# Performance work log

Measured on AMD Instinct MI355X. Metric: run time of the kernel, lower is better.

Reference implementation:

```python
import jax, jax.numpy as jnp
import numpy as np

B, T, D = 4, 2048, 768
H, HD = 8, 96          # n_heads, head_dim
NB = HD // 24          # number of 24-dim Leech blocks per head
NEG_INF = -1e30


def _leech_kernel_24():
    # QR of the bidiagonal/circulant base matrix, as in generate_leech_kernel
    base = np.zeros((24, 24), dtype=np.float32)
    for i in range(23):
        base[i, i] = 2.0
        base[i, i + 1] = 2.0
    base[23, 23] = 2.0
    base[23, 0] = -2.0
    q, _ = np.linalg.qr(base)
    return jnp.asarray(q, dtype=jnp.float32)


def setup_inputs() -> dict:
    key = jax.random.key(0)
    k1, k2, k3 = jax.random.split(key, 3)
    x = jax.random.normal(k1, (B, T, D), dtype=jnp.float32)
    w_qkv = jax.random.normal(k2, (3 * D, D), dtype=jnp.float32) * (D ** -0.5)
    w_out = jax.random.normal(k3, (D, D), dtype=jnp.float32) * (D ** -0.5)
    kernel = _leech_kernel_24()
    return {"x": x, "w_qkv": w_qkv, "w_out": w_out, "kernel": kernel}


def reference(x, w_qkv, w_out, kernel):
    Bx, Tx, Dx = x.shape
    scale = HD ** -0.5
    # qkv projection (bias=False)
    qkv = jnp.einsum('btd,ed->bte', x, w_qkv)            # [B,T,3D]
    qkv = qkv.reshape(Bx, Tx, 3, H, HD).transpose(2, 0, 3, 1, 4)  # [3,B,H,T,HD]
    q, k, v = qkv[0], qkv[1], qkv[2]
    # per-24-block orthogonal Leech rotation on q and k
    q = jnp.einsum('bhtni,ij->bhtnj', q.reshape(Bx, H, Tx, NB, 24), kernel)
    k = jnp.einsum('bhtni,ij->bhtnj', k.reshape(Bx, H, Tx, NB, 24), kernel)
    q = q.reshape(Bx, H, Tx, HD)
    k = k.reshape(Bx, H, Tx, HD)
    # causal attention (manual softmax; dropout inactive in eval)
    scores = jnp.einsum('bhqd,bhkd->bhqk', q, k) * scale
    causal = jnp.tril(jnp.ones((Tx, Tx), dtype=bool))
    scores = jnp.where(causal[None, None], scores, NEG_INF)
    attn = jax.nn.softmax(scores, axis=-1)
    out = jnp.einsum('bhqk,bhkd->bhqd', attn, v)          # [B,H,T,HD]
    out = out.transpose(0, 2, 1, 3).reshape(Bx, Tx, Dx)
    return jnp.einsum('btd,ed->bte', out, w_out)
```

## Files before the change

kernel.cpp:

```cpp
#include <hip/hip_runtime.h>
#include <cstdint>
#include <cstddef>

#define Bq 4
#define T 2048
#define Dm 768
#define H 8
#define HD 96
#define BH 32
#define QEL ((size_t)BH*T*HD)
#define KEL ((size_t)BH*T*128)
#define PSTRIDE 98304
#define QS 0.14724703336f
#define KVB 64
#define M0 12.0f

typedef unsigned int u32;
typedef unsigned long long u64;
typedef _Float16 f16x8 __attribute__((ext_vector_type(8)));
typedef _Float16 f16x4 __attribute__((ext_vector_type(4)));
typedef float f32x4 __attribute__((ext_vector_type(4)));

__global__ __launch_bounds__(256)
void cvt_tile(const float* __restrict__ in, _Float16* __restrict__ out)
{
    const int tid  = threadIdx.x;
    const int lane = tid & 63;
    const int gw   = (blockIdx.x * 256 + tid) >> 6;
    const int kc   = gw % 96;
    const int row  = (gw / 96) * 64 + lane;
    const float4 a = *reinterpret_cast<const float4*>(in + (size_t)row * 768 + kc * 8);
    const float4 b = *reinterpret_cast<const float4*>(in + (size_t)row * 768 + kc * 8 + 4);
    f16x8 h;
    h[0] = (_Float16)a.x; h[1] = (_Float16)a.y; h[2] = (_Float16)a.z; h[3] = (_Float16)a.w;
    h[4] = (_Float16)b.x; h[5] = (_Float16)b.y; h[6] = (_Float16)b.z; h[7] = (_Float16)b.w;
    *reinterpret_cast<f16x8*>(
        out + (size_t)(row >> 7) * PSTRIDE + (size_t)kc * 1024 + (row & 127) * 8) = h;
}

template <bool SCATTER>
__global__ __launch_bounds__(256)
void gemm_mfma(const _Float16* __restrict__ At, const _Float16* __restrict__ Bt,
               _Float16* __restrict__ qb, _Float16* __restrict__ kpd,
               _Float16* __restrict__ vtb, float* __restrict__ C,
               int N, int nx)
{
    __shared__ _Float16 As[8 * 128 * 8];
    __shared__ _Float16 Bs[8 * 128 * 8];

    const int tid  = threadIdx.x;
    const int lane = tid & 63;
    const int wid  = tid >> 6;
    const int li   = lane & 15;
    const int lg   = lane >> 4;
    const int wr   = wid >> 1;
    const int wc   = wid & 1;

    const int qch = gridDim.x >> 3;
    const int id  = (blockIdx.x & 7) * qch + (blockIdx.x >> 3);
    const int m0  = (id / nx) * 128;
    const int n0  = (id % nx) * 128;

    const _Float16* baseA = At + (size_t)(m0 >> 7) * PSTRIDE;
    const _Float16* baseB = Bt + (size_t)(n0 >> 7) * PSTRIDE;

    f32x4 acc[4][4];
#pragma unroll
    for (int i = 0; i < 4; ++i)
#pragma unroll
        for (int j = 0; j < 4; ++j) acc[i][j] = (f32x4)0.f;

    for (int k0 = 0; k0 < Dm; k0 += 64) {
        const _Float16* pa = baseA + (k0 >> 3) * 1024;
        const _Float16* pb = baseB + (k0 >> 3) * 1024;
#pragma unroll
        for (int i = 0; i < 4; ++i) {
            const int s = wid * 64 + i * 256;
            __builtin_amdgcn_global_load_lds(
                (const __attribute__((address_space(1))) void*)(pa + (size_t)(s + lane) * 8),
                (__attribute__((address_space(3))) void*)&As[s * 8], 16, 0, 0);
            __builtin_amdgcn_global_load_lds(
                (const __attribute__((address_space(1))) void*)(pb + (size_t)(s + lane) * 8),
                (__attribute__((address_space(3))) void*)&Bs[s * 8], 16, 0, 0);
        }
        __syncthreads();

#pragma unroll
        for (int c = 0; c < 2; ++c) {
            f16x8 af[4], bf[4];
#pragma unroll
            for (int i = 0; i < 4; ++i)
                af[i] = *reinterpret_cast<const f16x8*>(
                    &As[((c * 4 + lg) * 128 + wr * 64 + i * 16 + li) * 8]);
#pragma unroll
            for (int j = 0; j < 4; ++j)
                bf[j] = *reinterpret_cast<const f16x8*>(
                    &Bs[((c * 4 + lg) * 128 + wc * 64 + j * 16 + li) * 8]);
#pragma unroll
            for (int i = 0; i < 4; ++i)
#pragma unroll
                for (int j = 0; j < 4; ++j)
                    acc[i][j] = __builtin_amdgcn_mfma_f32_16x16x32_f16(
                        af[i], bf[j], acc[i][j], 0, 0, 0);
        }
        __syncthreads();
    }

#pragma unroll
    for (int i = 0; i < 4; ++i) {
#pragma unroll
        for (int r = 0; r < 4; ++r) {
            const int m = m0 + wr * 64 + i * 16 + lg * 4 + r;
            if (SCATTER) {
                const int b_ = m >> 11, t_ = m & 2047;
#pragma unroll
                for (int j = 0; j < 4; ++j) {
                    const int e = n0 + wc * 64 + j * 16 + li;
                    const int c = e / Dm;
                    const int rem = e - c * Dm;
                    const int h = rem / HD;
                    const int d = rem - h * HD;
                    const size_t bhx = (size_t)(b_ * H + h);
                    const float v = acc[i][j][r];
                    if (c == 0)
                        qb[(bhx * T + t_) * HD + d] = (_Float16)(v * QS);
                    else if (c == 1)
                        kpd[(bhx * T + t_) * 128 + d] = (_Float16)v;
                    else
                        vtb[(bhx * 96 + d) * T + t_] = (_Float16)v;
                }
            } else {
#pragma unroll
                for (int j = 0; j < 4; ++j) {
                    const int n = n0 + wc * 64 + j * 16 + li;
                    C[(size_t)m * N + n] = acc[i][j][r];
                }
            }
        }
    }
}

__global__ __launch_bounds__(256)
void attn_mfma(const _Float16* __restrict__ QG, const _Float16* __restrict__ KG,
               const _Float16* __restrict__ VtG, _Float16* __restrict__ aoh)
{
    __shared__ __align__(16) _Float16 Klds[2][64 * 128];
    __shared__ __align__(16) _Float16 Vlds[2][112 * 64];
    __shared__ __align__(16) _Float16 Pl[4][16][72];

    const int tid  = threadIdx.x;
    const int lane = tid & 63;
    const int wid  = tid >> 6;
    const int lg   = lane >> 4;
    const int li   = lane & 15;

    const int bh = blockIdx.x & 31;
    const int i  = blockIdx.x >> 5;
    const int qt0 = i, qt1 = 31 - i;

    {
        const u32 one2 = 0x3C003C00u;
        u32* vp0 = reinterpret_cast<u32*>(&Vlds[0][96 * 64]);
        u32* vp1 = reinterpret_cast<u32*>(&Vlds[1][96 * 64]);
#pragma unroll
        for (int k = tid; k < 512; k += 256) {
            const u32 v = (k < 32) ? one2 : 0u;
            vp0[k] = v; vp1[k] = v;
        }
    }
    __syncthreads();

    f16x8 qf0[3], qf1[3];
    {
        const _Float16* qr0 = QG + ((size_t)bh * T + qt0 * 64 + wid * 16 + li) * HD;
        const _Float16* qr1 = QG + ((size_t)bh * T + qt1 * 64 + wid * 16 + li) * HD;
#pragma unroll
        for (int ch = 0; ch < 3; ++ch) {
            qf0[ch] = *reinterpret_cast<const f16x8*>(qr0 + ch * 32 + lg * 8);
            qf1[ch] = *reinterpret_cast<const f16x8*>(qr1 + ch * 32 + lg * 8);
        }
    }

    const int swz = (li & 7) << 3;
    int kofs[4][3], vofs[7][2];
#pragma unroll
    for (int kt = 0; kt < 4; ++kt)
#pragma unroll
        for (int ch = 0; ch < 3; ++ch)
            kofs[kt][ch] = (kt * 16 + li) * 128 + ((ch * 32 + lg * 8) ^ swz);
#pragma unroll
    for (int dt = 0; dt < 7; ++dt)
#pragma unroll
        for (int pc = 0; pc < 2; ++pc)
            vofs[dt][pc] = (dt * 16 + li) * 64 + ((pc * 32 + lg * 8) ^ swz);

    const int rK = lane >> 4;
    const int cK = (lane & 15) * 8;
    const int rV = lane >> 3;
    const int cV = (lane & 7) * 8;
    auto STAGE = [&](int kb, int b) {
#pragma unroll
        for (int ii = 0; ii < 4; ++ii) {
            const int r  = wid * 16 + ii * 4 + rK;
            const int c0 = cK ^ (((ii * 4 + rK) & 7) << 3);
            const _Float16* src = KG + ((size_t)(bh * T + kb + r)) * 128 + c0;
            __builtin_amdgcn_global_load_lds(
                (const __attribute__((address_space(1))) void*)src,
                (__attribute__((address_space(3))) void*)&Klds[b][(wid * 16 + ii * 4) * 128],
                16, 0, 0);
        }
#pragma unroll
        for (int jj = 0; jj < 3; ++jj) {
            const int r  = wid * 24 + jj * 8 + rV;
            const int c0 = cV ^ (rV << 3);
            const _Float16* src = VtG + ((size_t)(bh * 96 + r)) * T + kb + c0;
            __builtin_amdgcn_global_load_lds(
                (const __attribute__((address_space(1))) void*)src,
                (__attribute__((address_space(3))) void*)&Vlds[b][(wid * 24 + jj * 8) * 64],
                16, 0, 0);
        }
    };

    f32x4 acc0[7], acc1[7];
#pragma unroll
    for (int dt = 0; dt < 7; ++dt) { acc0[dt] = (f32x4)0.f; acc1[dt] = (f32x4)0.f; }

    auto ROUND_FULL = [&](const f16x8 (&qf)[3], f32x4 (&acc)[7],
                          int p, int nextkb) {
        STAGE(nextkb, p ^ 1);
        asm volatile("s_waitcnt vmcnt(7)" ::: "memory");
        __builtin_amdgcn_s_barrier();

        const _Float16* Kb = &Klds[p][0];
        const _Float16* Vb = &Vlds[p][0];

        f16x8 kf[4][3];
#pragma unroll
        for (int kt = 0; kt < 4; ++kt)
#pragma unroll
            for (int ch = 0; ch < 3; ++ch)
                kf[kt][ch] = *reinterpret_cast<const f16x8*>(Kb + kofs[kt][ch]);

        f32x4 st[4];
        __builtin_amdgcn_s_setprio(1);
#pragma unroll
        for (int kt = 0; kt < 4; ++kt) {
            st[kt] = (f32x4)(-M0);
#pragma unroll
            for (int ch = 0; ch < 3; ++ch)
                st[kt] = __builtin_amdgcn_mfma_f32_16x16x32_f16(
                    kf[kt][ch], qf[ch], st[kt], 0, 0, 0);
        }
        __builtin_amdgcn_s_setprio(0);

#pragma unroll
        for (int kt = 0; kt < 4; ++kt) {
            const auto a = __builtin_amdgcn_cvt_pkrtz(
                __builtin_amdgcn_exp2f(st[kt][0]),
                __builtin_amdgcn_exp2f(st[kt][1]));
            const auto b = __builtin_amdgcn_cvt_pkrtz(
                __builtin_amdgcn_exp2f(st[kt][2]),
                __builtin_amdgcn_exp2f(st[kt][3]));
            const u64 w = (u64)__builtin_bit_cast(u32, a) |
                          ((u64)__builtin_bit_cast(u32, b) << 32);
            *reinterpret_cast<u64*>(&Pl[wid][li][kt * 16 + lg * 4]) = w;
        }

#pragma unroll
        for (int pc = 0; pc < 2; ++pc) {
            const f16x8 pf = *reinterpret_cast<const f16x8*>(
                &Pl[wid][li][pc * 32 + lg * 8]);
            __builtin_amdgcn_s_setprio(1);
#pragma unroll
            for (int dt = 0; dt < 7; ++dt) {
                const f16x8 vf = *reinterpret_cast<const f16x8*>(Vb + vofs[dt][pc]);
                acc[dt] = __builtin_amdgcn_mfma_f32_16x16x32_f16(
                    pf, vf, acc[dt], 0, 0, 0);
            }
            __builtin_amdgcn_s_setprio(0);
        }

        asm volatile("s_waitcnt lgkmcnt(0)" ::: "memory");
        __builtin_amdgcn_s_barrier();
    };

    auto ROUND_DIAG = [&](int kb, int q0w, const f16x8 (&qf)[3], f32x4 (&acc)[7],
                          int p, int nextkb, bool has_next) {
        if (has_next) {
            STAGE(nextkb, p ^ 1);
            asm volatile("s_waitcnt vmcnt(7)" ::: "memory");
        } else {
            asm volatile("s_waitcnt vmcnt(0)" ::: "memory");
        }
        __builtin_amdgcn_s_barrier();

        const _Float16* Kb = &Klds[p][0];
        const _Float16* Vb = &Vlds[p][0];
        const int nkt = min(4, ((q0w + 15 - kb) >> 4) + 1);

        f16x8 kf[4][3];
#pragma unroll
        for (int kt = 0; kt < 4; ++kt)
            if (kt < nkt) {
#pragma unroll
                for (int ch = 0; ch < 3; ++ch)
                    kf[kt][ch] = *reinterpret_cast<const f16x8*>(Kb + kofs[kt][ch]);
            }

        f32x4 st[4];
        __builtin_amdgcn_s_setprio(1);
#pragma unroll
        for (int kt = 0; kt < 4; ++kt) {
            st[kt] = (f32x4)(-M0);
            if (kt < nkt) {
#pragma unroll
                for (int ch = 0; ch < 3; ++ch)
                    st[kt] = __builtin_amdgcn_mfma_f32_16x16x32_f16(
                        kf[kt][ch], qf[ch], st[kt], 0, 0, 0);
            }
        }
        __builtin_amdgcn_s_setprio(0);

        const int qg = q0w + li;
#pragma unroll
        for (int kt = 0; kt < 4; ++kt)
            if (kt < nkt && kb + kt * 16 + 15 > q0w) {
#pragma unroll
                for (int rr = 0; rr < 4; ++rr) {
                    const int kg = kb + kt * 16 + lg * 4 + rr;
                    if (kg > qg) st[kt][rr] = -1e30f;
                }
            }

#pragma unroll
        for (int kt = 0; kt < 4; ++kt)
            if (kt < nkt) {
                const auto a = __builtin_amdgcn_cvt_pkrtz(
                    __builtin_amdgcn_exp2f(st[kt][0]),
                    __builtin_amdgcn_exp2f(st[kt][1]));
                const auto b = __builtin_amdgcn_cvt_pkrtz(
                    __builtin_amdgcn_exp2f(st[kt][2]),
                    __builtin_amdgcn_exp2f(st[kt][3]));
                const u64 w = (u64)__builtin_bit_cast(u32, a) |
                              ((u64)__builtin_bit_cast(u32, b) << 32);
                *reinterpret_cast<u64*>(&Pl[wid][li][kt * 16 + lg * 4]) = w;
            }
        if (nkt & 1)
            *reinterpret_cast<u64*>(&Pl[wid][li][nkt * 16 + lg * 4]) = 0ull;

        const int npc = (nkt + 1) >> 1;
#pragma unroll
        for (int pc = 0; pc < 2; ++pc)
            if (pc < npc) {
                const f16x8 pf = *reinterpret_cast<const f16x8*>(
                    &Pl[wid][li][pc * 32 + lg * 8]);
                __builtin_amdgcn_s_setprio(1);
#pragma unroll
                for (int dt = 0; dt < 7; ++dt) {
                    const f16x8 vf = *reinterpret_cast<const f16x8*>(Vb + vofs[dt][pc]);
                    acc[dt] = __builtin_amdgcn_mfma_f32_16x16x32_f16(
                        pf, vf, acc[dt], 0, 0, 0);
                }
                __builtin_amdgcn_s_setprio(0);
            }

        asm volatile("s_waitcnt lgkmcnt(0)" ::: "memory");
        __builtin_amdgcn_s_barrier();
    };

    STAGE(0, 0);
    const int q0w0 = qt0 * 64 + wid * 16;
    const int q0w1 = qt1 * 64 + wid * 16;
    int r = 0;
    for (int t = 0; t < i; ++t, ++r)
        ROUND_FULL(qf0, acc0, r & 1, (t + 1) * KVB);
    ROUND_DIAG(i * KVB, q0w0, qf0, acc0, r & 1, 0, true); ++r;
    for (int t = 0; t < 31 - i; ++t, ++r)
        ROUND_FULL(qf1, acc1, r & 1, (t + 1) * KVB);
    ROUND_DIAG((31 - i) * KVB, q0w1, qf1, acc1, r & 1, 0, false);

    const int ob = bh >> 3, oh = bh & 7;
#pragma unroll
    for (int rr = 0; rr < 4; ++rr) {
        {
            const float l    = __shfl(acc0[6][rr], lg << 4);
            const float linv = 1.0f / l;
            const int m = ob * T + qt0 * 64 + wid * 16 + lg * 4 + rr;
            _Float16* op = aoh + (size_t)(m >> 7) * PSTRIDE + (size_t)(m & 127) * 8
                         + (size_t)(oh * 12 + (li >> 3)) * 1024 + (li & 7);
#pragma unroll
            for (int dt = 0; dt < 6; ++dt)
                op[dt * 2048] = (_Float16)(acc0[dt][rr] * linv);
        }
        {
            const float l    = __shfl(acc1[6][rr], lg << 4);
            const float linv = 1.0f / l;
            const int m = ob * T + qt1 * 64 + wid * 16 + lg * 4 + rr;
            _Float16* op = aoh + (size_t)(m >> 7) * PSTRIDE + (size_t)(m & 127) * 8
                         + (size_t)(oh * 12 + (li >> 3)) * 1024 + (li & 7);
#pragma unroll
            for (int dt = 0; dt < 6; ++dt)
                op[dt * 2048] = (_Float16)(acc1[dt][rr] * linv);
        }
    }
}

extern "C" void kernel_launch(void* const* d_in, const int* in_sizes, int n_in,
                              void* d_out, int out_size, void* d_ws, size_t ws_size,
                              hipStream_t stream)
{
    const float* x     = (const float*)d_in[0];
    const float* w_qkv = (const float*)d_in[1];
    const float* w_out = (const float*)d_in[2];

    _Float16* qb  = (_Float16*)d_ws;
    _Float16* kpd = qb + QEL;
    _Float16* vtb = kpd + KEL;
    _Float16* aoh = vtb + QEL;
    _Float16* xh  = aoh + (size_t)Bq * T * Dm;
    _Float16* wqh = xh + (size_t)Bq * T * Dm;
    _Float16* woh = wqh + (size_t)3 * Dm * Dm;
    float* out = (float*)d_out;

    const int M = Bq * T;

    cvt_tile<<<dim3(M * 96 / 256), dim3(256), 0, stream>>>(x, xh);
    cvt_tile<<<dim3(3 * Dm * 96 / 256), dim3(256), 0, stream>>>(w_qkv, wqh);
    cvt_tile<<<dim3(Dm * 96 / 256), dim3(256), 0, stream>>>(w_out, woh);

    gemm_mfma<true><<<dim3((3 * Dm / 128) * (M / 128)), dim3(256), 0, stream>>>(
        xh, wqh, qb, kpd, vtb, nullptr, 3 * Dm, 3 * Dm / 128);

    attn_mfma<<<dim3(BH * (T / 128)), dim3(256), 0, stream>>>(qb, kpd, vtb, aoh);

    gemm_mfma<false><<<dim3((Dm / 128) * (M / 128)), dim3(256), 0, stream>>>(
        aoh, woh, nullptr, nullptr, nullptr, out, Dm, Dm / 128);
}
```

Baseline: 153.6 us.

## Double-buffer GEMM LDS tiles with async prefetch and MFMA priority boost

```diff
diff --git a/kernel.cpp b/kernel.cpp
--- a/kernel.cpp
+++ b/kernel.cpp
@@ -45,8 +45,9 @@
                _Float16* __restrict__ vtb, float* __restrict__ C,
                int N, int nx)
 {
-    __shared__ _Float16 As[8 * 128 * 8];
-    __shared__ _Float16 Bs[8 * 128 * 8];
+    constexpr int NSTEP = Dm / 64;
+    __shared__ _Float16 As[2][8 * 128 * 8];
+    __shared__ _Float16 Bs[2][8 * 128 * 8];
 
     const int tid  = threadIdx.x;
     const int lane = tid & 63;
@@ -70,20 +71,31 @@
 #pragma unroll
         for (int j = 0; j < 4; ++j) acc[i][j] = (f32x4)0.f;
 
-    for (int k0 = 0; k0 < Dm; k0 += 64) {
-        const _Float16* pa = baseA + (k0 >> 3) * 1024;
-        const _Float16* pb = baseB + (k0 >> 3) * 1024;
+    auto STAGE = [&](int t, int b) {
+        const _Float16* pa = baseA + (t << 13);
+        const _Float16* pb = baseB + (t << 13);
 #pragma unroll
         for (int i = 0; i < 4; ++i) {
             const int s = wid * 64 + i * 256;
             __builtin_amdgcn_global_load_lds(
                 (const __attribute__((address_space(1))) void*)(pa + (size_t)(s + lane) * 8),
-                (__attribute__((address_space(3))) void*)&As[s * 8], 16, 0, 0);
+                (__attribute__((address_space(3))) void*)&As[b][s * 8], 16, 0, 0);
             __builtin_amdgcn_global_load_lds(
                 (const __attribute__((address_space(1))) void*)(pb + (size_t)(s + lane) * 8),
-                (__attribute__((address_space(3))) void*)&Bs[s * 8], 16, 0, 0);
-        }
-        __syncthreads();
+                (__attribute__((address_space(3))) void*)&Bs[b][s * 8], 16, 0, 0);
+        }
+    };
+
+    STAGE(0, 0);
+    for (int t = 0; t < NSTEP; ++t) {
+        const int p = t & 1;
+        if (t + 1 < NSTEP) {
+            STAGE(t + 1, p ^ 1);
+            asm volatile("s_waitcnt vmcnt(8)" ::: "memory");
+        } else {
+            asm volatile("s_waitcnt vmcnt(0)" ::: "memory");
+        }
+        __builtin_amdgcn_s_barrier();
 
 #pragma unroll
         for (int c = 0; c < 2; ++c) {
@@ -91,19 +103,23 @@
 #pragma unroll
             for (int i = 0; i < 4; ++i)
                 af[i] = *reinterpret_cast<const f16x8*>(
-                    &As[((c * 4 + lg) * 128 + wr * 64 + i * 16 + li) * 8]);
+                    &As[p][((c * 4 + lg) * 128 + wr * 64 + i * 16 + li) * 8]);
 #pragma unroll
             for (int j = 0; j < 4; ++j)
                 bf[j] = *reinterpret_cast<const f16x8*>(
-                    &Bs[((c * 4 + lg) * 128 + wc * 64 + j * 16 + li) * 8]);
+                    &Bs[p][((c * 4 + lg) * 128 + wc * 64 + j * 16 + li) * 8]);
+            __builtin_amdgcn_s_setprio(1);
 #pragma unroll
             for (int i = 0; i < 4; ++i)
 #pragma unroll
                 for (int j = 0; j < 4; ++j)
                     acc[i][j] = __builtin_amdgcn_mfma_f32_16x16x32_f16(
                         af[i], bf[j], acc[i][j], 0, 0, 0);
-        }
-        __syncthreads();
+            __builtin_amdgcn_s_setprio(0);
+        }
+
+        asm volatile("s_waitcnt lgkmcnt(0)" ::: "memory");
+        __builtin_amdgcn_s_barrier();
     }
 
 #pragma unroll
```

After: 148.0 us. 3.6% less time.
